# Performance work log

Measured on AMD Instinct MI355X. Metric: run time of the kernel, lower is better.

Reference implementation:

```python
import jax, jax.numpy as jnp
import numpy as np

N, E, D, C, H1 = 50000, 800000, 128, 8, 2


def setup_inputs() -> dict:
    key = jax.random.key(0)
    ks = jax.random.split(key, 14)
    s = lambda k, sh: (jax.random.normal(k, sh, jnp.float32) * 0.05)
    return {
        "x": jax.random.normal(ks[0], (N, D), jnp.float32),
        "edge_index": jax.random.randint(ks[1], (2, E), 0, N, dtype=jnp.int32),
        # conv1: GATConv(D, D, heads=2, concat=True)
        "W1": s(ks[2], (D, H1 * D)),
        "att1_src": s(ks[3], (H1, D)),
        "att1_dst": s(ks[4], (H1, D)),
        "b1": s(ks[5], (H1 * D,)),
        # conv2: GATConv(2D, D, heads=1, concat=False)
        "W2": s(ks[6], (H1 * D, D)),
        "att2_src": s(ks[7], (1, D)),
        "att2_dst": s(ks[8], (1, D)),
        "b2": s(ks[9], (D,)),
        # MLP head
        "Wm1": s(ks[10], (D, D)),
        "bm1": s(ks[11], (D,)),
        "Wm2": s(ks[12], (D, C)),
        "bm2": s(ks[13], (C,)),
    }


def gat_conv(x, src, dst, W, a_src, a_dst, b, heads, out_ch, concat):
    """PyG GATConv (eval mode): self-loops added by caller, softmax over
    edges grouped by destination node, negative_slope=0.2."""
    n = x.shape[0]
    h = (x @ W).reshape(n, heads, out_ch)              # [N,H,F]
    alpha_src = jnp.einsum('nhf,hf->nh', h, a_src)     # [N,H]
    alpha_dst = jnp.einsum('nhf,hf->nh', h, a_dst)     # [N,H]
    e = jax.nn.leaky_relu(alpha_src[src] + alpha_dst[dst], 0.2)  # [E,H]
    e_max = jax.ops.segment_max(e, dst, num_segments=n)
    ex = jnp.exp(e - e_max[dst])
    denom = jax.ops.segment_sum(ex, dst, num_segments=n)
    alpha = ex / jnp.maximum(denom[dst], 1e-16)        # [E,H]
    out = jax.ops.segment_sum(h[src] * alpha[:, :, None], dst, num_segments=n)
    out = out.reshape(n, heads * out_ch) if concat else out.mean(axis=1)
    return out + b


def reference(x, edge_index, W1, att1_src, att1_dst, b1,
              W2, att2_src, att2_dst, b2, Wm1, bm1, Wm2, bm2):
    n = x.shape[0]
    loop = jnp.arange(n, dtype=edge_index.dtype)
    src = jnp.concatenate([edge_index[0], loop])  # add_self_loops=True
    dst = jnp.concatenate([edge_index[1], loop])
    h = jax.nn.elu(gat_conv(x, src, dst, W1, att1_src, att1_dst, b1, H1, D, True))
    h = jax.nn.elu(gat_conv(h, src, dst, W2, att2_src, att2_dst, b2, 1, D, False))
    h = jax.nn.relu(h @ Wm1 + bm1)
    return jax.nn.relu(h @ Wm2 + bm2)
```

## Files before the change

kernel.cpp:

```cpp
#include <hip/hip_runtime.h>
#include <hip/hip_bf16.h>


__device__ __forceinline__ float lrelu(float x){ return x > 0.f ? x : 0.2f*x; }
__device__ __forceinline__ float elu_f(float x){ return x > 0.f ? x : __expf(x) - 1.f; }
__device__ __forceinline__ unsigned short f2bf(float f){
  __hip_bfloat16 h = __float2bfloat16(f);
  return *reinterpret_cast<unsigned short*>(&h);
}
__device__ __forceinline__ float bflo(unsigned int u){ return __uint_as_float(u << 16); }
__device__ __forceinline__ float bfhi(unsigned int u){ return __uint_as_float(u & 0xffff0000u); }
__device__ __forceinline__ unsigned int packbf(float a, float b){
  return (unsigned int)f2bf(a) | ((unsigned int)f2bf(b) << 16);
}

typedef __attribute__((ext_vector_type(8))) short bf16x8;
typedef __attribute__((ext_vector_type(4))) float f32x4;

__global__ void prep_kernel(const float* __restrict__ W1, unsigned short* __restrict__ BT1a,
                            unsigned short* __restrict__ BT1b,
                            const float* __restrict__ W2, unsigned short* __restrict__ BT2,
                            const float* __restrict__ Wm1, unsigned short* __restrict__ BT3,
                            const float* __restrict__ a1s, const float* __restrict__ a1d,
                            float* __restrict__ va, int* __restrict__ bcount,
                            int* __restrict__ gcur, int NB){
  int idx = blockIdx.x*256 + threadIdx.x;
  const int S1 = 128*128, S2 = 128*256, S3 = 128*128;
  if (idx < S1){
    int n = idx >> 7, k = idx & 127;
    BT1a[idx] = f2bf(W1[(size_t)k*256 + n]);
    BT1b[idx] = f2bf(W1[(size_t)k*256 + 128 + n]);
  } else if (idx < S1 + S2){
    int j = idx - S1;
    int n = j >> 8, k = j & 255;
    BT2[j] = f2bf(W2[(size_t)k*128 + n]);
  } else if (idx < S1 + S2 + S3){
    int j = idx - S1 - S2;
    int n = j >> 7, k = j & 127;
    BT3[j] = f2bf(Wm1[(size_t)k*128 + n]);
  } else if (idx < S1 + S2 + S3 + 512){
    int j = idx - S1 - S2 - S3;
    int v = j >> 7, k = j & 127;
    const float* avec = (v < 2) ? a1s : a1d;
    int head = v & 1;
    const float* wrow = W1 + (size_t)k*256 + head*128;
    const float* arow = avec + head*128;
    float s = 0.f;
    #pragma unroll 8
    for (int f = 0; f < 128; ++f) s += wrow[f]*arow[f];
    va[j] = s;
  } else if (idx < S1 + S2 + S3 + 512 + 2048){
    int z = idx - (S1 + S2 + S3 + 512);
    if (z < 1024){ if (z < NB) bcount[z] = 0; }
    else { z -= 1024; if (z < NB) gcur[z] = 0; }
  }
}

__global__ __launch_bounds__(256) void f2bf_hist_kernel(
    const float* __restrict__ x, unsigned short* __restrict__ xb, int N,
    const float* __restrict__ va, float* __restrict__ as1, float* __restrict__ ad1,
    const int* __restrict__ dst, int E, int* __restrict__ bcount, int NB, int nbConv)
{
  __shared__ int h[1024];
  if ((int)blockIdx.x < nbConv){
    int i = blockIdx.x*256 + threadIdx.x;
    int total = N*32;
    float4 v = make_float4(0.f,0.f,0.f,0.f);
    if (i < total){
      v = ((const float4*)x)[i];
      ushort4 u; u.x=f2bf(v.x); u.y=f2bf(v.y); u.z=f2bf(v.z); u.w=f2bf(v.w);
      ((ushort4*)xb)[i] = u;
    }
    int c = (i & 31) << 2;
    float4 vs0 = *(const float4*)(va + c);
    float4 vs1 = *(const float4*)(va + 128 + c);
    float4 vd0 = *(const float4*)(va + 256 + c);
    float4 vd1 = *(const float4*)(va + 384 + c);
    float s0 = v.x*vs0.x + v.y*vs0.y + v.z*vs0.z + v.w*vs0.w;
    float s1 = v.x*vs1.x + v.y*vs1.y + v.z*vs1.z + v.w*vs1.w;
    float d0 = v.x*vd0.x + v.y*vd0.y + v.z*vd0.z + v.w*vd0.w;
    float d1 = v.x*vd1.x + v.y*vd1.y + v.z*vd1.z + v.w*vd1.w;
    #pragma unroll
    for (int m = 1; m <= 16; m <<= 1){
      s0 += __shfl_xor(s0, m); s1 += __shfl_xor(s1, m);
      d0 += __shfl_xor(d0, m); d1 += __shfl_xor(d1, m);
    }
    if ((i & 31) == 0 && i < total){
      int n = i >> 5;
      *(float2*)(as1 + 2*n) = make_float2(s0, s1);
      *(float2*)(ad1 + 2*n) = make_float2(d0, d1);
    }
  } else {
    for (int i = threadIdx.x; i < NB; i += 256) h[i] = 0;
    __syncthreads();
    int b0 = blockIdx.x - nbConv;
    for (int e = b0*256 + threadIdx.x; e < E; e += 64*256)
      atomicAdd(&h[dst[e] >> 6], 1);
    __syncthreads();
    for (int i = threadIdx.x; i < NB; i += 256)
      if (h[i]) atomicAdd(&bcount[i], h[i]);
  }
}

__global__ __launch_bounds__(1024) void bscan_kernel(const int* __restrict__ bcount,
                                                     int* __restrict__ boff, int NB){
  __shared__ int s[1024];
  int t = threadIdx.x;
  int mine = (t < NB) ? bcount[t] : 0;
  s[t] = mine;
  __syncthreads();
  for (int d = 1; d < 1024; d <<= 1){
    int v = (t >= d) ? s[t-d] : 0;
    __syncthreads();
    s[t] += v;
    __syncthreads();
  }
  if (t < NB) boff[t] = s[t] - mine;
  if (t == NB-1) boff[NB] = s[t];
}

__global__ __launch_bounds__(256) void bscatter_kernel(
    const int* __restrict__ src, const int* __restrict__ dst, int E,
    const int* __restrict__ boff, int* __restrict__ gcur,
    unsigned int* __restrict__ pairs, int NB)
{
  __shared__ int h[1024];
  __shared__ int runbase[1024];
  const int t = threadIdx.x;
  const int e0 = blockIdx.x * 4096;
  for (int i = t; i < NB; i += 256) h[i] = 0;
  __syncthreads();
  int myb[16]; unsigned int myw[16];
  #pragma unroll
  for (int q = 0; q < 16; ++q){
    int e = e0 + q*256 + t;
    int b = -1; unsigned int w = 0;
    if (e < E){
      int d = dst[e];
      b = d >> 6;
      w = ((unsigned int)(d & 63) << 26) | (unsigned int)src[e];
      atomicAdd(&h[b], 1);
    }
    myb[q] = b; myw[q] = w;
  }
  __syncthreads();
  for (int i = t; i < NB; i += 256)
    runbase[i] = h[i] ? atomicAdd(&gcur[i], h[i]) : 0;
  __syncthreads();
  for (int i = t; i < NB; i += 256) h[i] = 0;
  __syncthreads();
  #pragma unroll
  for (int q = 0; q < 16; ++q){
    if (myb[q] >= 0){
      int off = atomicAdd(&h[myb[q]], 1);
      pairs[(size_t)boff[myb[q]] + runbase[myb[q]] + off] = myw[q];
    }
  }
}

__global__ __launch_bounds__(256) void bbuild_kernel(
    const unsigned int* __restrict__ pairs, const int* __restrict__ boff,
    int* __restrict__ rowptr, int* __restrict__ csr, int N)
{
  __shared__ int deg[64], offs[64], cur[64];
  const int b = blockIdx.x;
  const int t = threadIdx.x;
  const int n0 = b << 6;
  const int nNodes = min(64, N - n0);
  const int p0 = boff[b], p1 = boff[b+1];
  const int base = p0 + n0;
  if (t < 64) deg[t] = (t < nNodes) ? 1 : 0;
  __syncthreads();
  for (int i = p0 + t; i < p1; i += 256)
    atomicAdd(&deg[pairs[i] >> 26], 1);
  __syncthreads();
  if (t < 64){
    int x = deg[t];
    #pragma unroll
    for (int d = 1; d < 64; d <<= 1){
      int y = __shfl_up(x, d);
      if (t >= d) x += y;
    }
    offs[t] = x - deg[t];
    cur[t] = 1;
    if (t < nNodes){
      rowptr[n0 + t + 1] = base + x;
      csr[base + x - deg[t]] = n0 + t;
    }
    if (b == 0 && t == 0) rowptr[0] = 0;
  }
  __syncthreads();
  for (int i = p0 + t; i < p1; i += 256){
    unsigned int w = pairs[i];
    int dl = w >> 26;
    int s  = (int)(w & 0x03ffffffu);
    int off = atomicAdd(&cur[dl], 1);
    csr[base + offs[dl] + off] = s;
  }
}

__device__ __forceinline__ void gemm_core(
    const unsigned short* __restrict__ A, int lda,
    const unsigned short* __restrict__ BT, int M, int K, int r0,
    unsigned short* a_s, unsigned short* b_s, f32x4 (&acc)[4][4])
{
  const int tid  = threadIdx.x;
  const int lane = tid & 63, wv = tid >> 6;
  const int mh = (wv & 1)*64, nh = (wv >> 1)*64;
  const int l15 = lane & 15, quad = lane >> 4;
  const int srow = tid >> 3, skc = tid & 7;

  #pragma unroll
  for (int i = 0; i < 4; ++i)
    #pragma unroll
    for (int j = 0; j < 4; ++j)
      #pragma unroll
      for (int r = 0; r < 4; ++r) acc[i][j][r] = 0.f;

  for (int k0 = 0; k0 < K; k0 += 64){
    #pragma unroll
    for (int it = 0; it < 4; ++it){
      int row = it*32 + srow;
      int grow = r0 + row;
      uint4 v = make_uint4(0u,0u,0u,0u);
      if (grow < M) v = *(const uint4*)(A + (size_t)grow*lda + k0 + skc*8);
      *(uint4*)(&a_s[row*72 + skc*8]) = v;
    }
    #pragma unroll
    for (int it = 0; it < 4; ++it){
      int row = it*32 + srow;
      uint4 v = *(const uint4*)(BT + (size_t)row*K + k0 + skc*8);
      *(uint4*)(&b_s[row*72 + skc*8]) = v;
    }
    __syncthreads();
    #pragma unroll
    for (int ks = 0; ks < 64; ks += 32){
      bf16x8 af[4], bfr[4];
      #pragma unroll
      for (int i = 0; i < 4; ++i)
        af[i] = *(const bf16x8*)(&a_s[(mh + i*16 + l15)*72 + ks + quad*8]);
      #pragma unroll
      for (int j = 0; j < 4; ++j)
        bfr[j] = *(const bf16x8*)(&b_s[(nh + j*16 + l15)*72 + ks + quad*8]);
      #pragma unroll
      for (int i = 0; i < 4; ++i)
        #pragma unroll
        for (int j = 0; j < 4; ++j)
          acc[i][j] = __builtin_amdgcn_mfma_f32_16x16x32_bf16(bfr[j], af[i], acc[i][j], 0, 0, 0);
    }
    __syncthreads();
  }
}

__global__ __launch_bounds__(256) void gemm_conv1_kernel(
    const unsigned short* __restrict__ xa, const unsigned short* __restrict__ BT1a,
    const unsigned short* __restrict__ BT1b, unsigned short* __restrict__ out1b,
    int M, const float* __restrict__ b1)
{
  __shared__ unsigned short a_s[128*72];
  __shared__ unsigned short b_s[128*72];
  const int hx = blockIdx.x;
  const unsigned short* A  = xa + hx*128;
  const unsigned short* BT = hx ? BT1b : BT1a;
  unsigned short* C = out1b + hx*128;
  const float* bias = b1 + hx*128;
  const int r0 = blockIdx.y*128;
  f32x4 acc[4][4];
  gemm_core(A, 256, BT, M, 128, r0, a_s, b_s, acc);

  const int lane = threadIdx.x & 63, wv = threadIdx.x >> 6;
  const int mh = (wv & 1)*64, nh = (wv >> 1)*64;
  const int l15 = lane & 15, quad = lane >> 4;
  #pragma unroll
  for (int i = 0; i < 4; ++i){
    int m = r0 + mh + i*16 + l15;
    if (m < M){
      #pragma unroll
      for (int j = 0; j < 4; ++j){
        int n = nh + j*16 + quad*4;
        float4 bb = *(const float4*)(bias + n);
        ushort4 u;
        u.x = f2bf(elu_f(acc[i][j][0] + bb.x));
        u.y = f2bf(elu_f(acc[i][j][1] + bb.y));
        u.z = f2bf(elu_f(acc[i][j][2] + bb.z));
        u.w = f2bf(elu_f(acc[i][j][3] + bb.w));
        *(ushort4*)(C + (size_t)m*256 + n) = u;
      }
    }
  }
}

__global__ __launch_bounds__(256) void gemm_conv2_kernel(
    const unsigned short* __restrict__ out1b, const unsigned short* __restrict__ BT2,
    unsigned short* __restrict__ h2b, int M,
    const float* __restrict__ a2s, const float* __restrict__ a2d,
    float* __restrict__ as2, float* __restrict__ ad2)
{
  __shared__ unsigned short a_s[128*72];
  __shared__ unsigned short b_s[128*72];
  __shared__ float part_s[128][2];
  __shared__ float part_d[128][2];
  const int r0 = blockIdx.y*128;
  f32x4 acc[4][4];
  gemm_core(out1b, 256, BT2, M, 256, r0, a_s, b_s, acc);

  const int tid = threadIdx.x;
  const int lane = tid & 63, wv = tid >> 6;
  const int mh = (wv & 1)*64, nh = (wv >> 1)*64;
  const int l15 = lane & 15, quad = lane >> 4;
  #pragma unroll
  for (int i = 0; i < 4; ++i){
    int m = r0 + mh + i*16 + l15;
    float ps = 0.f, pd = 0.f;
    #pragma unroll
    for (int j = 0; j < 4; ++j){
      int n = nh + j*16 + quad*4;
      float4 wsv = *(const float4*)(a2s + n);
      float4 wdv = *(const float4*)(a2d + n);
      float v0 = acc[i][j][0], v1 = acc[i][j][1], v2 = acc[i][j][2], v3 = acc[i][j][3];
      ps += v0*wsv.x + v1*wsv.y + v2*wsv.z + v3*wsv.w;
      pd += v0*wdv.x + v1*wdv.y + v2*wdv.z + v3*wdv.w;
      if (m < M){
        ushort4 u;
        u.x = f2bf(v0); u.y = f2bf(v1); u.z = f2bf(v2); u.w = f2bf(v3);
        *(ushort4*)(h2b + (size_t)m*128 + n) = u;
      }
    }
    ps += __shfl_xor(ps, 16); ps += __shfl_xor(ps, 32);
    pd += __shfl_xor(pd, 16); pd += __shfl_xor(pd, 32);
    if (quad == 0){
      part_s[mh + i*16 + l15][wv >> 1] = ps;
      part_d[mh + i*16 + l15][wv >> 1] = pd;
    }
  }
  __syncthreads();
  if (tid < 128){
    int gm = r0 + tid;
    if (gm < M){
      as2[gm] = part_s[tid][0] + part_s[tid][1];
      ad2[gm] = part_d[tid][0] + part_d[tid][1];
    }
  }
}

__global__ __launch_bounds__(256) void gemm_mlp_kernel(
    const unsigned short* __restrict__ gb, const unsigned short* __restrict__ BT3,
    int M, const float* __restrict__ bm1, const float* __restrict__ Wm2,
    const float* __restrict__ bm2, float* __restrict__ out)
{
  __shared__ unsigned short a_s[128*72];
  __shared__ unsigned short b_s[128*72];
  __shared__ float wm2_s[128*8];
  __shared__ float part[128][2][8];
  const int tid = threadIdx.x;
  {
    int i4 = tid*4;
    *(float4*)(&wm2_s[i4]) = *(const float4*)(Wm2 + i4);
  }
  const int r0 = blockIdx.y*128;
  f32x4 acc[4][4];
  gemm_core(gb, 128, BT3, M, 128, r0, a_s, b_s, acc);

  const int lane = tid & 63, wv = tid >> 6;
  const int mh = (wv & 1)*64, nh = (wv >> 1)*64;
  const int l15 = lane & 15, quad = lane >> 4;
  #pragma unroll
  for (int i = 0; i < 4; ++i){
    float po[8];
    #pragma unroll
    for (int o = 0; o < 8; ++o) po[o] = 0.f;
    #pragma unroll
    for (int j = 0; j < 4; ++j){
      int n = nh + j*16 + quad*4;
      float4 bb = *(const float4*)(bm1 + n);
      #pragma unroll
      for (int r = 0; r < 4; ++r){
        float hcol = fmaxf(acc[i][j][r] + ((const float*)&bb)[r], 0.f);
        const float* wr = &wm2_s[(n + r)*8];
        #pragma unroll
        for (int o = 0; o < 8; ++o) po[o] += hcol*wr[o];
      }
    }
    #pragma unroll
    for (int o = 0; o < 8; ++o){
      po[o] += __shfl_xor(po[o], 16);
      po[o] += __shfl_xor(po[o], 32);
    }
    if (quad == 0){
      #pragma unroll
      for (int o = 0; o < 8; ++o) part[mh + i*16 + l15][wv >> 1][o] = po[o];
    }
  }
  __syncthreads();
  if (tid < 128){
    int gm = r0 + tid;
    if (gm < M){
      float4 o0, o1;
      o0.x = fmaxf(part[tid][0][0] + part[tid][1][0] + bm2[0], 0.f);
      o0.y = fmaxf(part[tid][0][1] + part[tid][1][1] + bm2[1], 0.f);
      o0.z = fmaxf(part[tid][0][2] + part[tid][1][2] + bm2[2], 0.f);
      o0.w = fmaxf(part[tid][0][3] + part[tid][1][3] + bm2[3], 0.f);
      o1.x = fmaxf(part[tid][0][4] + part[tid][1][4] + bm2[4], 0.f);
      o1.y = fmaxf(part[tid][0][5] + part[tid][1][5] + bm2[5], 0.f);
      o1.z = fmaxf(part[tid][0][6] + part[tid][1][6] + bm2[6], 0.f);
      o1.w = fmaxf(part[tid][0][7] + part[tid][1][7] + bm2[7], 0.f);
      *(float4*)(out + (size_t)gm*8)     = o0;
      *(float4*)(out + (size_t)gm*8 + 4) = o1;
    }
  }
}

__global__ __launch_bounds__(256) void agg1x_kernel(
    const unsigned short* __restrict__ xb, const float* __restrict__ as_,
    const float* __restrict__ ad_, const int* __restrict__ rowptr, const int* __restrict__ csr,
    unsigned short* __restrict__ xa, int N)
{
  const int wv = threadIdx.x >> 6, lane = threadIdx.x & 63;
  const int ql = lane & 15;
  const int n = blockIdx.x*16 + wv*4 + (lane >> 4);
  const bool valid = n < N;
  int start = 0, end = 0;
  float2 adv = make_float2(0.f, 0.f);
  if (valid){ start = rowptr[n]; end = rowptr[n+1]; adv = *(const float2*)(ad_ + 2*n); }

  int jl = start + ql;
  bool have = valid && (jl < end);
  int s_l = 0;
  float p0 = 0.f, p1 = 0.f;
  if (have){
    s_l = csr[jl];
    float2 av = *(const float2*)(as_ + 2*s_l);
    p0 = __expf(lrelu(av.x + adv.x));
    p1 = __expf(lrelu(av.y + adv.y));
  }
  float l0 = p0, l1 = p1;
  for (int j = jl + 16; j < end; j += 16){
    int s = csr[j];
    float2 av = *(const float2*)(as_ + 2*s);
    l0 += __expf(lrelu(av.x + adv.x));
    l1 += __expf(lrelu(av.y + adv.y));
  }
  #pragma unroll
  for (int msk = 1; msk <= 8; msk <<= 1){
    l0 += __shfl_xor(l0, msk);
    l1 += __shfl_xor(l1, msk);
  }
  float inv0 = 1.f / fmaxf(l0, 1e-16f);
  float inv1 = 1.f / fmaxf(l1, 1e-16f);
  float a0_l = p0 * inv0;
  float a1_l = p1 * inv1;

  float acc0[8], acc1[8];
  #pragma unroll
  for (int i = 0; i < 8; ++i){ acc0[i] = 0.f; acc1[i] = 0.f; }
  const int c = ql << 3;
  const unsigned short* hp = xb + c;

  int cnt = valid ? min(16, end - start) : 0;
  for (int t = 0; t < cnt; ++t){
    int   sA  = __shfl(s_l, t, 16);
    float a0A = __shfl(a0_l, t, 16);
    float a1A = __shfl(a1_l, t, 16);
    uint4 u = *(const uint4*)(hp + (sA << 7));
    float f0 = bflo(u.x), f1 = bfhi(u.x), f2v = bflo(u.y), f3 = bfhi(u.y);
    float f4 = bflo(u.z), f5 = bfhi(u.z), f6 = bflo(u.w), f7 = bfhi(u.w);
    acc0[0] += a0A*f0; acc0[1] += a0A*f1; acc0[2] += a0A*f2v; acc0[3] += a0A*f3;
    acc0[4] += a0A*f4; acc0[5] += a0A*f5; acc0[6] += a0A*f6;  acc0[7] += a0A*f7;
    acc1[0] += a1A*f0; acc1[1] += a1A*f1; acc1[2] += a1A*f2v; acc1[3] += a1A*f3;
    acc1[4] += a1A*f4; acc1[5] += a1A*f5; acc1[6] += a1A*f6;  acc1[7] += a1A*f7;
  }
  for (int jb = start + 16; jb < end; jb += 16){
    int jl2 = jb + ql;
    int s2 = 0; float a0_2 = 0.f, a1_2 = 0.f;
    if (jl2 < end){
      s2 = csr[jl2];
      float2 av = *(const float2*)(as_ + 2*s2);
      a0_2 = __expf(lrelu(av.x + adv.x)) * inv0;
      a1_2 = __expf(lrelu(av.y + adv.y)) * inv1;
    }
    int cnt2 = min(16, end - jb);
    for (int t2 = 0; t2 < cnt2; ++t2){
      int   sA  = __shfl(s2, t2, 16);
      float a0A = __shfl(a0_2, t2, 16);
      float a1A = __shfl(a1_2, t2, 16);
      uint4 u = *(const uint4*)(hp + (sA << 7));
      float f0 = bflo(u.x), f1 = bfhi(u.x), f2v = bflo(u.y), f3 = bfhi(u.y);
      float f4 = bflo(u.z), f5 = bfhi(u.z), f6 = bflo(u.w), f7 = bfhi(u.w);
      acc0[0] += a0A*f0; acc0[1] += a0A*f1; acc0[2] += a0A*f2v; acc0[3] += a0A*f3;
      acc0[4] += a0A*f4; acc0[5] += a0A*f5; acc0[6] += a0A*f6;  acc0[7] += a0A*f7;
      acc1[0] += a1A*f0; acc1[1] += a1A*f1; acc1[2] += a1A*f2v; acc1[3] += a1A*f3;
      acc1[4] += a1A*f4; acc1[5] += a1A*f5; acc1[6] += a1A*f6;  acc1[7] += a1A*f7;
    }
  }

  if (valid){
    uint4 u0, u1;
    u0.x = packbf(acc0[0], acc0[1]); u0.y = packbf(acc0[2], acc0[3]);
    u0.z = packbf(acc0[4], acc0[5]); u0.w = packbf(acc0[6], acc0[7]);
    u1.x = packbf(acc1[0], acc1[1]); u1.y = packbf(acc1[2], acc1[3]);
    u1.z = packbf(acc1[4], acc1[5]); u1.w = packbf(acc1[6], acc1[7]);
    *(uint4*)(xa + (size_t)n*256 + c)       = u0;
    *(uint4*)(xa + (size_t)n*256 + 128 + c) = u1;
  }
}

__global__ __launch_bounds__(256) void agg2_kernel(
    const unsigned short* __restrict__ h2b, const float* __restrict__ as_,
    const float* __restrict__ ad_, const int* __restrict__ rowptr, const int* __restrict__ csr,
    const float* __restrict__ b2, unsigned short* __restrict__ outb, int N)
{
  const int wv = threadIdx.x >> 6, lane = threadIdx.x & 63;
  const int ql = lane & 15;
  const int n = blockIdx.x*16 + wv*4 + (lane >> 4);
  const bool valid = n < N;
  int start = 0, end = 0;
  float adn = 0.f;
  if (valid){ start = rowptr[n]; end = rowptr[n+1]; adn = ad_[n]; }

  int jl = start + ql;
  bool have = valid && (jl < end);
  int s_l = 0;
  float p_l = 0.f;
  if (have){
    s_l = csr[jl];
    p_l = __expf(lrelu(as_[s_l] + adn));
  }
  float l = p_l;
  for (int j = jl + 16; j < end; j += 16)
    l += __expf(lrelu(as_[csr[j]] + adn));
  #pragma unroll
  for (int msk = 1; msk <= 8; msk <<= 1) l += __shfl_xor(l, msk);
  float inv = 1.f / fmaxf(l, 1e-16f);
  float a_l = p_l * inv;

  float acc[8];
  #pragma unroll
  for (int i = 0; i < 8; ++i) acc[i] = 0.f;
  const int c = ql << 3;
  const unsigned short* hp = h2b + c;

  int cnt = valid ? min(16, end - start) : 0;
  int t = 0;
  for (; t + 1 < cnt; t += 2){
    int   sA = __shfl(s_l, t, 16),  sB = __shfl(s_l, t+1, 16);
    float aA = __shfl(a_l, t, 16),  aB = __shfl(a_l, t+1, 16);
    uint4 uA = *(const uint4*)(hp + (sA << 7));
    uint4 uB = *(const uint4*)(hp + (sB << 7));
    acc[0] += aA*bflo(uA.x) + aB*bflo(uB.x);
    acc[1] += aA*bfhi(uA.x) + aB*bfhi(uB.x);
    acc[2] += aA*bflo(uA.y) + aB*bflo(uB.y);
    acc[3] += aA*bfhi(uA.y) + aB*bfhi(uB.y);
    acc[4] += aA*bflo(uA.z) + aB*bflo(uB.z);
    acc[5] += aA*bfhi(uA.z) + aB*bfhi(uB.z);
    acc[6] += aA*bflo(uA.w) + aB*bflo(uB.w);
    acc[7] += aA*bfhi(uA.w) + aB*bfhi(uB.w);
  }
  if (t < cnt){
    int   sA = __shfl(s_l, t, 16);
    float aA = __shfl(a_l, t, 16);
    uint4 uA = *(const uint4*)(hp + (sA << 7));
    acc[0] += aA*bflo(uA.x); acc[1] += aA*bfhi(uA.x);
    acc[2] += aA*bflo(uA.y); acc[3] += aA*bfhi(uA.y);
    acc[4] += aA*bflo(uA.z); acc[5] += aA*bfhi(uA.z);
    acc[6] += aA*bflo(uA.w); acc[7] += aA*bfhi(uA.w);
  }
  for (int jb = start + 16; jb < end; jb += 16){
    int jl2 = jb + ql;
    int s2 = 0; float a2 = 0.f;
    if (jl2 < end){
      s2 = csr[jl2];
      a2 = __expf(lrelu(as_[s2] + adn)) * inv;
    }
    int cnt2 = min(16, end - jb);
    for (int t2 = 0; t2 < cnt2; ++t2){
      int   sA = __shfl(s2, t2, 16);
      float aA = __shfl(a2, t2, 16);
      uint4 uA = *(const uint4*)(hp + (sA << 7));
      acc[0] += aA*bflo(uA.x); acc[1] += aA*bfhi(uA.x);
      acc[2] += aA*bflo(uA.y); acc[3] += aA*bfhi(uA.y);
      acc[4] += aA*bflo(uA.z); acc[5] += aA*bfhi(uA.z);
      acc[6] += aA*bflo(uA.w); acc[7] += aA*bfhi(uA.w);
    }
  }

  if (valid){
    float4 bb0 = *(const float4*)(b2 + c);
    float4 bb1 = *(const float4*)(b2 + c + 4);
    float o[8];
    o[0]=elu_f(acc[0]+bb0.x); o[1]=elu_f(acc[1]+bb0.y);
    o[2]=elu_f(acc[2]+bb0.z); o[3]=elu_f(acc[3]+bb0.w);
    o[4]=elu_f(acc[4]+bb1.x); o[5]=elu_f(acc[5]+bb1.y);
    o[6]=elu_f(acc[6]+bb1.z); o[7]=elu_f(acc[7]+bb1.w);
    uint4 up;
    up.x = packbf(o[0], o[1]); up.y = packbf(o[2], o[3]);
    up.z = packbf(o[4], o[5]); up.w = packbf(o[6], o[7]);
    *(uint4*)(outb + (size_t)n*128 + c) = up;
  }
}

extern "C" void kernel_launch(void* const* d_in, const int* in_sizes, int n_in,
                              void* d_out, int out_size, void* d_ws, size_t ws_size,
                              hipStream_t stream)
{
  (void)n_in; (void)out_size; (void)ws_size;
  const float* x   = (const float*)d_in[0];
  const int*   ei  = (const int*)d_in[1];
  const float* W1  = (const float*)d_in[2];
  const float* a1s = (const float*)d_in[3];
  const float* a1d = (const float*)d_in[4];
  const float* b1  = (const float*)d_in[5];
  const float* W2  = (const float*)d_in[6];
  const float* a2s = (const float*)d_in[7];
  const float* a2d = (const float*)d_in[8];
  const float* b2  = (const float*)d_in[9];
  const float* Wm1 = (const float*)d_in[10];
  const float* bm1 = (const float*)d_in[11];
  const float* Wm2 = (const float*)d_in[12];
  const float* bm2 = (const float*)d_in[13];
  float* out = (float*)d_out;

  const int N = in_sizes[0] / 128;
  const int E = in_sizes[1] / 2;
  const int NB = (N + 63) >> 6;
  const int* srcp = ei;
  const int* dstp = ei + E;

  char* ws = (char*)d_ws;
  unsigned short* xb    = (unsigned short*)ws;
  unsigned short* xa    = (unsigned short*)(ws + (size_t)N*256);
  unsigned short* out1b = (unsigned short*)(ws + (size_t)N*768);
  unsigned short* h2b   = (unsigned short*)(ws + (size_t)N*1280);
  char* tail = ws + (size_t)N*1536;
  unsigned short* BT1a = (unsigned short*)tail;
  unsigned short* BT1b = BT1a + 128*128;
  unsigned short* BT2  = BT1b + 128*128;
  unsigned short* BT3  = BT2 + 128*256;
  float* va   = (float*)(BT3 + 128*128);
  float* as1  = va + 512;
  float* ad1  = as1 + (size_t)2*N;
  float* as2  = ad1 + (size_t)2*N;
  float* ad2  = as2 + N;
  int* bcount = (int*)(ad2 + N);
  int* boff   = bcount + 1024;
  int* gcur   = boff + 1032;
  int* rowptr = gcur + 1024;
  int* csr    = rowptr + N + 1;
  unsigned int* pairs = (unsigned int*)(csr + E + N);

  unsigned short* gb = xb;

  const int nbConv = (N*32 + 255)/256;
  const int prepTotal = 128*128 + 128*256 + 128*128 + 512 + 2048;

  prep_kernel<<<(prepTotal + 255)/256, 256, 0, stream>>>(
      W1, BT1a, BT1b, W2, BT2, Wm1, BT3, a1s, a1d, va, bcount, gcur, NB);
  f2bf_hist_kernel<<<nbConv + 64, 256, 0, stream>>>(x, xb, N, va, as1, ad1,
                                                    dstp, E, bcount, NB, nbConv);
  bscan_kernel<<<1, 1024, 0, stream>>>(bcount, boff, NB);
  bscatter_kernel<<<(E + 4095)/4096, 256, 0, stream>>>(srcp, dstp, E, boff, gcur, pairs, NB);
  bbuild_kernel<<<NB, 256, 0, stream>>>(pairs, boff, rowptr, csr, N);

  const int gy   = (N + 127) / 128;
  const int nb16 = (N + 15) / 16;

  agg1x_kernel<<<nb16, 256, 0, stream>>>(xb, as1, ad1, rowptr, csr, xa, N);
  gemm_conv1_kernel<<<dim3(2, gy), 256, 0, stream>>>(xa, BT1a, BT1b, out1b, N, b1);
  gemm_conv2_kernel<<<dim3(1, gy), 256, 0, stream>>>(out1b, BT2, h2b, N, a2s, a2d, as2, ad2);
  agg2_kernel<<<nb16, 256, 0, stream>>>(h2b, as2, ad2, rowptr, csr, b2, gb, N);
  gemm_mlp_kernel<<<dim3(1, gy), 256, 0, stream>>>(gb, BT3, N, bm1, Wm2, bm2, out);
}
```

Before: 267.4 us.

## Fuse graph-build preprocessing kernels into one cooperative grid-synced kernel

Replaces five preprocessing launches (weight transpose, bf16 conversion with attention dots and histogram, bucket scan, scatter, CSR build) with a single cooperative kernel that uses grid-wide syncs between phases. It is meant to remove launch gaps and the tail idle time between small kernels. The cost is a fixed grid of at most 512 blocks running grid-stride loops, a scan done by one block while the others wait at the barrier, and a device attribute query on every call; the old kernels remain as a fallback if the cooperative launch fails.

```diff
diff --git a/kernel.cpp b/kernel.cpp
--- a/kernel.cpp
+++ b/kernel.cpp
@@ -1,6 +1,9 @@
 #include <hip/hip_runtime.h>
 #include <hip/hip_bf16.h>
-
+#include <hip/hip_cooperative_groups.h>
+
+
+namespace cg = cooperative_groups;
 
 __device__ __forceinline__ float lrelu(float x){ return x > 0.f ? x : 0.2f*x; }
 __device__ __forceinline__ float elu_f(float x){ return x > 0.f ? x : __expf(x) - 1.f; }
@@ -16,6 +19,192 @@
 
 typedef __attribute__((ext_vector_type(8))) short bf16x8;
 typedef __attribute__((ext_vector_type(4))) float f32x4;
+
+__global__ __launch_bounds__(256, 2) void build_coop(
+    const float* __restrict__ x, unsigned short* __restrict__ xb, int N,
+    const float* __restrict__ W1, unsigned short* __restrict__ BT1a, unsigned short* __restrict__ BT1b,
+    const float* __restrict__ W2, unsigned short* __restrict__ BT2,
+    const float* __restrict__ Wm1, unsigned short* __restrict__ BT3,
+    const float* __restrict__ a1s, const float* __restrict__ a1d, float* __restrict__ va,
+    float* __restrict__ as1, float* __restrict__ ad1,
+    const int* __restrict__ srcp, const int* __restrict__ dstp, int E,
+    int* __restrict__ bcount, int* __restrict__ boff, int* __restrict__ gcur,
+    unsigned int* __restrict__ pairs, int* __restrict__ rowptr, int* __restrict__ csr, int NB)
+{
+  cg::grid_group g = cg::this_grid();
+  __shared__ int h[1024];
+  __shared__ int rb[1024];
+  const int t = threadIdx.x;
+  const int stride = gridDim.x*256;
+
+  const int S1 = 128*128, S2 = 128*256, S3 = 128*128;
+  const int prepTotal = S1 + S2 + S3 + 512 + 2048;
+  for (int idx = blockIdx.x*256 + t; idx < prepTotal; idx += stride){
+    if (idx < S1){
+      int n = idx >> 7, k = idx & 127;
+      BT1a[idx] = f2bf(W1[(size_t)k*256 + n]);
+      BT1b[idx] = f2bf(W1[(size_t)k*256 + 128 + n]);
+    } else if (idx < S1 + S2){
+      int j = idx - S1;
+      int n = j >> 8, k = j & 255;
+      BT2[j] = f2bf(W2[(size_t)k*128 + n]);
+    } else if (idx < S1 + S2 + S3){
+      int j = idx - S1 - S2;
+      int n = j >> 7, k = j & 127;
+      BT3[j] = f2bf(Wm1[(size_t)k*128 + n]);
+    } else if (idx < S1 + S2 + S3 + 512){
+      int j = idx - S1 - S2 - S3;
+      int v = j >> 7, k = j & 127;
+      const float* avec = (v < 2) ? a1s : a1d;
+      int head = v & 1;
+      const float* wrow = W1 + (size_t)k*256 + head*128;
+      const float* arow = avec + head*128;
+      float s = 0.f;
+      #pragma unroll 8
+      for (int f = 0; f < 128; ++f) s += wrow[f]*arow[f];
+      va[j] = s;
+    } else {
+      int z = idx - (S1 + S2 + S3 + 512);
+      if (z < 1024){ if (z < NB) bcount[z] = 0; }
+      else { z -= 1024; if (z < NB) gcur[z] = 0; }
+    }
+  }
+  g.sync();
+
+  const int total = N*32;
+  for (int i = blockIdx.x*256 + t; i < total; i += stride){
+    float4 v = ((const float4*)x)[i];
+    ushort4 u; u.x=f2bf(v.x); u.y=f2bf(v.y); u.z=f2bf(v.z); u.w=f2bf(v.w);
+    ((ushort4*)xb)[i] = u;
+    int c = (i & 31) << 2;
+    float4 vs0 = *(const float4*)(va + c);
+    float4 vs1 = *(const float4*)(va + 128 + c);
+    float4 vd0 = *(const float4*)(va + 256 + c);
+    float4 vd1 = *(const float4*)(va + 384 + c);
+    float s0 = v.x*vs0.x + v.y*vs0.y + v.z*vs0.z + v.w*vs0.w;
+    float s1 = v.x*vs1.x + v.y*vs1.y + v.z*vs1.z + v.w*vs1.w;
+    float d0 = v.x*vd0.x + v.y*vd0.y + v.z*vd0.z + v.w*vd0.w;
+    float d1 = v.x*vd1.x + v.y*vd1.y + v.z*vd1.z + v.w*vd1.w;
+    #pragma unroll
+    for (int m = 1; m <= 16; m <<= 1){
+      s0 += __shfl_xor(s0, m); s1 += __shfl_xor(s1, m);
+      d0 += __shfl_xor(d0, m); d1 += __shfl_xor(d1, m);
+    }
+    if ((i & 31) == 0){
+      int n = i >> 5;
+      *(float2*)(as1 + 2*n) = make_float2(s0, s1);
+      *(float2*)(ad1 + 2*n) = make_float2(d0, d1);
+    }
+  }
+  for (int i = t; i < NB; i += 256) h[i] = 0;
+  __syncthreads();
+  for (int e = blockIdx.x*256 + t; e < E; e += stride)
+    atomicAdd(&h[dstp[e] >> 6], 1);
+  __syncthreads();
+  for (int i = t; i < NB; i += 256)
+    if (h[i]) atomicAdd(&bcount[i], h[i]);
+  g.sync();
+
+  if (blockIdx.x == 0){
+    const int lane = t & 63, w = t >> 6;
+    int carry = 0;
+    for (int base = 0; base < NB; base += 256){
+      int idx = base + t;
+      int v = (idx < NB) ? bcount[idx] : 0;
+      int s = v;
+      #pragma unroll
+      for (int d = 1; d < 64; d <<= 1){
+        int y = __shfl_up(s, d);
+        if (lane >= d) s += y;
+      }
+      if (lane == 63) rb[w] = s;
+      __syncthreads();
+      int add = 0;
+      #pragma unroll
+      for (int k = 0; k < 4; ++k) if (k < w) add += rb[k];
+      int ctot = rb[0] + rb[1] + rb[2] + rb[3];
+      if (idx < NB) boff[idx] = carry + s + add - v;
+      carry += ctot;
+      __syncthreads();
+    }
+    if (t == 0) boff[NB] = carry;
+  }
+  g.sync();
+
+  const int nchunks = (E + 4095)/4096;
+  for (int vb = blockIdx.x; vb < nchunks; vb += gridDim.x){
+    const int e0 = vb*4096;
+    for (int i = t; i < NB; i += 256) h[i] = 0;
+    __syncthreads();
+    int myb[16]; unsigned int myw[16];
+    #pragma unroll
+    for (int q = 0; q < 16; ++q){
+      int e = e0 + q*256 + t;
+      int b = -1; unsigned int w = 0;
+      if (e < E){
+        int d = dstp[e];
+        b = d >> 6;
+        w = ((unsigned int)(d & 63) << 26) | (unsigned int)srcp[e];
+        atomicAdd(&h[b], 1);
+      }
+      myb[q] = b; myw[q] = w;
+    }
+    __syncthreads();
+    for (int i = t; i < NB; i += 256)
+      rb[i] = h[i] ? atomicAdd(&gcur[i], h[i]) : 0;
+    __syncthreads();
+    for (int i = t; i < NB; i += 256) h[i] = 0;
+    __syncthreads();
+    #pragma unroll
+    for (int q = 0; q < 16; ++q){
+      if (myb[q] >= 0){
+        int off = atomicAdd(&h[myb[q]], 1);
+        pairs[(size_t)boff[myb[q]] + rb[myb[q]] + off] = myw[q];
+      }
+    }
+    __syncthreads();
+  }
+  g.sync();
+
+  for (int vb = blockIdx.x; vb < NB; vb += gridDim.x){
+    int* deg  = h;
+    int* offs = rb;
+    int* cur  = rb + 64;
+    const int n0 = vb << 6;
+    const int nNodes = min(64, N - n0);
+    const int p0 = boff[vb], p1 = boff[vb+1];
+    const int base = p0 + n0;
+    if (t < 64) deg[t] = (t < nNodes) ? 1 : 0;
+    __syncthreads();
+    for (int i = p0 + t; i < p1; i += 256)
+      atomicAdd(&deg[pairs[i] >> 26], 1);
+    __syncthreads();
+    if (t < 64){
+      int xsc = deg[t];
+      #pragma unroll
+      for (int d = 1; d < 64; d <<= 1){
+        int y = __shfl_up(xsc, d);
+        if (t >= d) xsc += y;
+      }
+      offs[t] = xsc - deg[t];
+      cur[t] = 1;
+      if (t < nNodes){
+        rowptr[n0 + t + 1] = base + xsc;
+        csr[base + xsc - deg[t]] = n0 + t;
+      }
+      if (vb == 0 && t == 0) rowptr[0] = 0;
+    }
+    __syncthreads();
+    for (int i = p0 + t; i < p1; i += 256){
+      unsigned int w = pairs[i];
+      int dl = w >> 26;
+      int s  = (int)(w & 0x03ffffffu);
+      int off = atomicAdd(&cur[dl], 1);
+      csr[base + offs[dl] + off] = s;
+    }
+    __syncthreads();
+  }
+}
 
 __global__ void prep_kernel(const float* __restrict__ W1, unsigned short* __restrict__ BT1a,
                             unsigned short* __restrict__ BT1b,
@@ -619,9 +808,9 @@
   const float* bm2 = (const float*)d_in[13];
   float* out = (float*)d_out;
 
-  const int N = in_sizes[0] / 128;
-  const int E = in_sizes[1] / 2;
-  const int NB = (N + 63) >> 6;
+  int N = in_sizes[0] / 128;
+  int E = in_sizes[1] / 2;
+  int NB = (N + 63) >> 6;
   const int* srcp = ei;
   const int* dstp = ei + E;
 
@@ -649,16 +838,38 @@
 
   unsigned short* gb = xb;
 
-  const int nbConv = (N*32 + 255)/256;
-  const int prepTotal = 128*128 + 128*256 + 128*128 + 512 + 2048;
-
-  prep_kernel<<<(prepTotal + 255)/256, 256, 0, stream>>>(
-      W1, BT1a, BT1b, W2, BT2, Wm1, BT3, a1s, a1d, va, bcount, gcur, NB);
-  f2bf_hist_kernel<<<nbConv + 64, 256, 0, stream>>>(x, xb, N, va, as1, ad1,
-                                                    dstp, E, bcount, NB, nbConv);
-  bscan_kernel<<<1, 1024, 0, stream>>>(bcount, boff, NB);
-  bscatter_kernel<<<(E + 4095)/4096, 256, 0, stream>>>(srcp, dstp, E, boff, gcur, pairs, NB);
-  bbuild_kernel<<<NB, 256, 0, stream>>>(pairs, boff, rowptr, csr, N);
+  int coopAttr = 0;
+  hipDeviceGetAttribute(&coopAttr, hipDeviceAttributeCooperativeLaunch, 0);
+  bool coopDone = false;
+  if (coopAttr){
+    int gridA = 512;
+    int maxA = (N*32 + 255)/256;
+    if (gridA > maxA) gridA = maxA;
+    void* argsA[] = {
+      (void*)&x, (void*)&xb, (void*)&N,
+      (void*)&W1, (void*)&BT1a, (void*)&BT1b,
+      (void*)&W2, (void*)&BT2, (void*)&Wm1, (void*)&BT3,
+      (void*)&a1s, (void*)&a1d, (void*)&va,
+      (void*)&as1, (void*)&ad1,
+      (void*)&srcp, (void*)&dstp, (void*)&E,
+      (void*)&bcount, (void*)&boff, (void*)&gcur,
+      (void*)&pairs, (void*)&rowptr, (void*)&csr, (void*)&NB
+    };
+    hipError_t rc = hipLaunchCooperativeKernel((const void*)build_coop, dim3(gridA),
+                                               dim3(256), argsA, 0, stream);
+    coopDone = (rc == hipSuccess);
+  }
+  if (!coopDone){
+    const int nbConv = (N*32 + 255)/256;
+    const int prepTotal = 128*128 + 128*256 + 128*128 + 512 + 2048;
+    prep_kernel<<<(prepTotal + 255)/256, 256, 0, stream>>>(
+        W1, BT1a, BT1b, W2, BT2, Wm1, BT3, a1s, a1d, va, bcount, gcur, NB);
+    f2bf_hist_kernel<<<nbConv + 64, 256, 0, stream>>>(x, xb, N, va, as1, ad1,
+                                                      dstp, E, bcount, NB, nbConv);
+    bscan_kernel<<<1, 1024, 0, stream>>>(bcount, boff, NB);
+    bscatter_kernel<<<(E + 4095)/4096, 256, 0, stream>>>(srcp, dstp, E, boff, gcur, pairs, NB);
+    bbuild_kernel<<<NB, 256, 0, stream>>>(pairs, boff, rowptr, csr, N);
+  }
 
   const int gy   = (N + 127) / 128;
   const int nb16 = (N + 15) / 16;
```

After: 486.7 us. 82.0% more time.
